# Optimization experiments

Measured on AMD Instinct MI355X. Metric: run time of the kernel, lower is better.

Reference implementation:

```python
import jax, jax.numpy as jnp
import numpy as np

NEG_INF = 1e10  # module's self.inf


def setup_inputs() -> dict:
    key = jax.random.key(0)
    k1, k2, k3, k4 = jax.random.split(key, 4)
    B, To, Ti, d = 16, 2048, 2048, 64
    q = jax.random.normal(k1, (B, To, d), dtype=jnp.float32)
    k = jax.random.normal(k2, (B, Ti, d), dtype=jnp.float32)
    v = jax.random.normal(k3, (B, Ti, d), dtype=jnp.float32)
    prod_mask = jax.random.randint(k4, (B, To, Ti), 0, 2, dtype=jnp.int32)
    return {"q": q, "k": k, "v": v, "prod_mask": prod_mask}


def reference(q, k, v, prod_mask):
    d_qk = q.shape[2]
    # [B, To, Ti] scores
    scaled_qk = jnp.einsum('bod,bid->boi', q, k) / jnp.sqrt(jnp.float32(d_qk))
    scaled_qk = jnp.where(prod_mask == 0, jnp.float32(-NEG_INF), scaled_qk)
    weights = jax.nn.softmax(scaled_qk, axis=2)
    # v flattened over trailing dims is already [B, Ti, d] here
    attended_v = jnp.einsum('boi,bid->bod', weights, v)
    return attended_v
```

## Files before the change

### kernel.cpp

```cpp
#include <hip/hip_runtime.h>
#include <stdint.h>

#define BATCH 16
#define TO 2048
#define TI 2048
#define DH 64
#define NITER2 16

typedef __attribute__((ext_vector_type(8))) short bf16x8;
typedef __attribute__((ext_vector_type(4))) float f32x4;

__device__ __forceinline__ unsigned short f2bf(float f) {
  uint32_t x = __float_as_uint(f);
  x += 0x7fffu + ((x >> 16) & 1u);
  return (unsigned short)(x >> 16);
}

__global__ __launch_bounds__(256) void convert_kv(
    const float* __restrict__ kg, const float* __restrict__ vg,
    unsigned short* __restrict__ k_bf, unsigned short* __restrict__ v_t) {
  __shared__ __align__(16) unsigned short vt[64][72];
  int b = blockIdx.y;
  int i0 = blockIdx.x * 64;
  int t = threadIdx.x;

  {
    const float4* src = (const float4*)(kg + ((size_t)b * TI + i0) * DH);
    ushort4* dst = (ushort4*)(k_bf + ((size_t)b * TI + i0) * DH);
#pragma unroll
    for (int u = 0; u < 4; ++u) {
      float4 f = src[t + 256 * u];
      ushort4 o;
      o.x = f2bf(f.x); o.y = f2bf(f.y); o.z = f2bf(f.z); o.w = f2bf(f.w);
      dst[t + 256 * u] = o;
    }
  }
  {
    const float4* src = (const float4*)(vg + ((size_t)b * TI + i0) * DH);
#pragma unroll
    for (int u = 0; u < 4; ++u) {
      int idx = t + 256 * u;
      int row = idx >> 4;
      int c4 = idx & 15;
      float4 f = src[idx];
      vt[c4 * 4 + 0][row] = f2bf(f.x);
      vt[c4 * 4 + 1][row] = f2bf(f.y);
      vt[c4 * 4 + 2][row] = f2bf(f.z);
      vt[c4 * 4 + 3][row] = f2bf(f.w);
    }
  }
  __syncthreads();
  {
    int dd = t >> 2, part = t & 3;
    ushort4* dst = (ushort4*)(v_t + ((size_t)b * DH + dd) * TI + i0 + part * 16);
#pragma unroll
    for (int u = 0; u < 4; ++u) {
      ushort4 o;
      o.x = vt[dd][part * 16 + u * 4 + 0];
      o.y = vt[dd][part * 16 + u * 4 + 1];
      o.z = vt[dd][part * 16 + u * 4 + 2];
      o.w = vt[dd][part * 16 + u * 4 + 3];
      dst[u] = o;
    }
  }
}

#define ATTN_BODY(IC, MCUR, MNXT)                                              \
  {                                                                            \
    if ((IC) < NITER2 - 1) {                                                   \
      _Pragma("unroll") for (int mt = 0; mt < 4; ++mt)                         \
          MNXT[mt] = *(const int4*)(mbase + mt * 16);                          \
      mbase += 64;                                                             \
    }                                                                          \
                                        \
    f32x4 st[4];                                                               \
    _Pragma("unroll") for (int mt = 0; mt < 4; ++mt) {                         \
      bf16x8 kf0 = *(const bf16x8*)&k_lds[g][mt * 16 + ln15][quad * 8];        \
      bf16x8 kf1 = *(const bf16x8*)&k_lds[g][mt * 16 + ln15][32 + quad * 8];   \
      f32x4 acc = (f32x4){0.f, 0.f, 0.f, 0.f};                                 \
      acc = __builtin_amdgcn_mfma_f32_16x16x32_bf16(kf0, qf[0], acc, 0, 0, 0); \
      acc = __builtin_amdgcn_mfma_f32_16x16x32_bf16(kf1, qf[1], acc, 0, 0, 0); \
      st[mt] = acc;                                                            \
    }                                                                          \
         \
    _Pragma("unroll") for (int mt = 0; mt < 4; ++mt) {                         \
      float p0 = (MCUR[mt].x != 0) ? __expf(st[mt][0]) : 0.f;                  \
      float p1 = (MCUR[mt].y != 0) ? __expf(st[mt][1]) : 0.f;                  \
      float p2 = (MCUR[mt].z != 0) ? __expf(st[mt][2]) : 0.f;                  \
      float p3 = (MCUR[mt].w != 0) ? __expf(st[mt][3]) : 0.f;                  \
      l_part += (p0 + p1) + (p2 + p3);                                         \
      uint32_t lo = (uint32_t)f2bf(p0) | ((uint32_t)f2bf(p1) << 16);           \
      uint32_t hi = (uint32_t)f2bf(p2) | ((uint32_t)f2bf(p3) << 16);           \
      uint2 pk; pk.x = lo; pk.y = hi;                                          \
      *(uint2*)&p_row[wave][ln15][mt * 16 + quad * 4] = pk;                    \
    }                                                                          \
            \
    bf16x8 pf0 = *(const bf16x8*)&p_row[wave][ln15][quad * 8];                 \
    bf16x8 pf1 = *(const bf16x8*)&p_row[wave][ln15][32 + quad * 8];            \
                                                         \
    _Pragma("unroll") for (int dt = 0; dt < 4; ++dt) {                         \
      bf16x8 vf0 = *(const bf16x8*)&v_lds[g][dt * 16 + ln15][quad * 8];        \
      bf16x8 vf1 = *(const bf16x8*)&v_lds[g][dt * 16 + ln15][32 + quad * 8];   \
      o_acc[dt] = __builtin_amdgcn_mfma_f32_16x16x32_bf16(vf0, pf0, o_acc[dt], 0, 0, 0); \
      o_acc[dt] = __builtin_amdgcn_mfma_f32_16x16x32_bf16(vf1, pf1, o_acc[dt], 0, 0, 0); \
    }                                                                          \
                                          \
    asm volatile("s_waitcnt lgkmcnt(0)\n\ts_barrier" ::: "memory");            \
    if ((IC) < NITER2 - 1) {                                                   \
                        \
      *(uint4*)&k_lds[g][row][part * 16] = ka0;                                \
      *(uint4*)&k_lds[g][row][part * 16 + 8] = ka1;                            \
      *(uint4*)&v_lds[g][row][part * 16] = va0;                                \
      *(uint4*)&v_lds[g][row][part * 16 + 8] = va1;                            \
               \
      if ((IC) < NITER2 - 2) {                                                 \
        ka0 = kp[0]; ka1 = kp[1];                                              \
        va0 = vp[0]; va1 = vp[1];                                              \
        kp = (const uint4*)((const char*)kp + 64 * DH * 2);                    \
        vp = (const uint4*)((const char*)vp + 64 * 2);                         \
      }                                                                        \
                                    \
      asm volatile("s_waitcnt lgkmcnt(0)\n\ts_barrier" ::: "memory");          \
    }                                                                          \
  }

__global__ __launch_bounds__(512) void attn_kernel(
    const float* __restrict__ q, const int* __restrict__ mask,
    const unsigned short* __restrict__ k_bf, const unsigned short* __restrict__ v_t,
    float* __restrict__ out) {
  __shared__ __align__(16) unsigned short k_lds[2][64][72];
  __shared__ __align__(16) unsigned short v_lds[2][64][72];
  __shared__ __align__(16) unsigned short p_row[8][16][72];

  int n = blockIdx.x;
  int xcd = n & 7;
  int slot = n >> 3;
  int b = (xcd << 1) | (slot >> 5);
  int o_blk = slot & 31;

  int t = threadIdx.x;
  int wave = t >> 6;
  int g = wave >> 2;
  int w = wave & 3;
  int lane = t & 63;
  int ln15 = lane & 15;
  int quad = lane >> 4;

  int qrow = o_blk * 64 + w * 16 + ln15;

  bf16x8 qf[2];
  {
    const float* qp = q + ((size_t)b * TO + qrow) * DH;
#pragma unroll
    for (int kc = 0; kc < 2; ++kc) {
      int kk = kc * 32 + quad * 8;
      float4 f0 = *(const float4*)(qp + kk);
      float4 f1 = *(const float4*)(qp + kk + 4);
      bf16x8 a;
      a[0] = (short)f2bf(f0.x * 0.125f);
      a[1] = (short)f2bf(f0.y * 0.125f);
      a[2] = (short)f2bf(f0.z * 0.125f);
      a[3] = (short)f2bf(f0.w * 0.125f);
      a[4] = (short)f2bf(f1.x * 0.125f);
      a[5] = (short)f2bf(f1.y * 0.125f);
      a[6] = (short)f2bf(f1.z * 0.125f);
      a[7] = (short)f2bf(f1.w * 0.125f);
      qf[kc] = a;
    }
  }

  f32x4 o_acc[4];
#pragma unroll
  for (int dt = 0; dt < 4; ++dt) o_acc[dt] = (f32x4){0.f, 0.f, 0.f, 0.f};
  float l_part = 0.f;

  int tg = t & 255;
  int row = tg >> 2, part = tg & 3;
  const uint4* kp = (const uint4*)(k_bf + ((size_t)b * TI + g * 1024 + row) * DH + part * 16);
  const uint4* vp = (const uint4*)(v_t + ((size_t)b * DH + row) * TI + g * 1024 + part * 16);
  const int* mbase = mask + ((size_t)b * TO + qrow) * TI + g * 1024 + quad * 4;

  uint4 ka0 = kp[0], ka1 = kp[1];
  uint4 va0 = vp[0], va1 = vp[1];
  kp = (const uint4*)((const char*)kp + 64 * DH * 2);
  vp = (const uint4*)((const char*)vp + 64 * 2);
  *(uint4*)&k_lds[g][row][part * 16] = ka0;
  *(uint4*)&k_lds[g][row][part * 16 + 8] = ka1;
  *(uint4*)&v_lds[g][row][part * 16] = va0;
  *(uint4*)&v_lds[g][row][part * 16 + 8] = va1;
  ka0 = kp[0]; ka1 = kp[1];
  va0 = vp[0]; va1 = vp[1];
  kp = (const uint4*)((const char*)kp + 64 * DH * 2);
  vp = (const uint4*)((const char*)vp + 64 * 2);
  int4 mv[4], mw[4];
#pragma unroll
  for (int mt = 0; mt < 4; ++mt) mv[mt] = *(const int4*)(mbase + mt * 16);
  mbase += 64;
  asm volatile("s_waitcnt lgkmcnt(0)\n\ts_barrier" ::: "memory");

  for (int ic = 0; ic < NITER2; ic += 2) {
    ATTN_BODY(ic, mv, mw)
    ATTN_BODY(ic + 1, mw, mv)
  }

  l_part += __shfl_xor(l_part, 16);
  l_part += __shfl_xor(l_part, 32);

  float* scr = (float*)&k_lds[0][0][0];
  float* lscr = (float*)&p_row[0][0][0];
  int orow_i = w * 16 + ln15;

  if (g == 1) {
#pragma unroll
    for (int dt = 0; dt < 4; ++dt)
      *(f32x4*)&scr[(size_t)orow_i * 68 + dt * 16 + quad * 4] = o_acc[dt];
    if (quad == 0) lscr[orow_i] = l_part;
  }
  asm volatile("s_waitcnt lgkmcnt(0)\n\ts_barrier" ::: "memory");
  if (g == 0) {
    float inv = 1.0f / (l_part + lscr[orow_i]);
    float* orow = out + ((size_t)b * TO + qrow) * DH;
#pragma unroll
    for (int dt = 0; dt < 4; ++dt) {
      f32x4 other = *(const f32x4*)&scr[(size_t)orow_i * 68 + dt * 16 + quad * 4];
      float4 vout;
      vout.x = (o_acc[dt][0] + other[0]) * inv;
      vout.y = (o_acc[dt][1] + other[1]) * inv;
      vout.z = (o_acc[dt][2] + other[2]) * inv;
      vout.w = (o_acc[dt][3] + other[3]) * inv;
      *(float4*)(orow + dt * 16 + quad * 4) = vout;
    }
  }
}

extern "C" void kernel_launch(void* const* d_in, const int* in_sizes, int n_in,
                              void* d_out, int out_size, void* d_ws, size_t ws_size,
                              hipStream_t stream) {
  const float* q = (const float*)d_in[0];
  const float* k = (const float*)d_in[1];
  const float* v = (const float*)d_in[2];
  const int* mask = (const int*)d_in[3];

  unsigned short* k_bf = (unsigned short*)d_ws;
  unsigned short* v_t = k_bf + (size_t)BATCH * TI * DH;

  convert_kv<<<dim3(TI / 64, BATCH), 256, 0, stream>>>(k, v, k_bf, v_t);
  attn_kernel<<<dim3(TO / 64 * BATCH), 512, 0, stream>>>(q, mask, k_bf, v_t, (float*)d_out);
}
```

Before: 90.86 us.

## Double-buffer K/V tiles in LDS with XOR swizzle, one barrier per step

Makes the K and V shared-memory tiles double-buffered, so the next tile is written into the other buffer while the current one is read. This drops the second barrier per iteration and moves the global prefetch earlier. It replaces the padded 72-wide rows with a 64-wide XOR-swizzled layout for K, V and P, keeping bank-conflict avoidance while using less LDS, and adds a min-blocks hint to launch bounds. LDS use grows from the extra buffer, and the launch-bounds hint may constrain register allocation.

```diff
diff --git a/kernel.cpp b/kernel.cpp
--- a/kernel.cpp
+++ b/kernel.cpp
@@ -65,18 +65,36 @@
   }
 }
 
-#define ATTN_BODY(IC, MCUR, MNXT)                                              \
+#define ATTN_BODY(CUR, IC, MCUR, MNXT)                                         \
   {                                                                            \
     if ((IC) < NITER2 - 1) {                                                   \
       _Pragma("unroll") for (int mt = 0; mt < 4; ++mt)                         \
           MNXT[mt] = *(const int4*)(mbase + mt * 16);                          \
       mbase += 64;                                                             \
-    }                                                                          \
-                                        \
+         \
+      {                                                                        \
+        unsigned short* kd = &k_lds[g][(CUR) ^ 1][row][0];                     \
+        unsigned short* vd = &v_lds[g][(CUR) ^ 1][row][0];                     \
+        int h = row & 7;                                                       \
+        *(uint4*)(kd + ((((2 * part) ^ h) << 3))) = ka0;                       \
+        *(uint4*)(kd + ((((2 * part + 1) ^ h) << 3))) = ka1;                   \
+        *(uint4*)(vd + ((((2 * part) ^ h) << 3))) = va0;                       \
+        *(uint4*)(vd + ((((2 * part + 1) ^ h) << 3))) = va1;                   \
+      }                                                                        \
+    }                                                                          \
+                \
+    if ((IC) < NITER2 - 2) {                                                   \
+      ka0 = kp[0]; ka1 = kp[1];                                                \
+      va0 = vp[0]; va1 = vp[1];                                                \
+      kp = (const uint4*)((const char*)kp + 64 * DH * 2);                      \
+      vp = (const uint4*)((const char*)vp + 64 * 2);                           \
+    }                                                                          \
+                 \
     f32x4 st[4];                                                               \
     _Pragma("unroll") for (int mt = 0; mt < 4; ++mt) {                         \
-      bf16x8 kf0 = *(const bf16x8*)&k_lds[g][mt * 16 + ln15][quad * 8];        \
-      bf16x8 kf1 = *(const bf16x8*)&k_lds[g][mt * 16 + ln15][32 + quad * 8];   \
+      const unsigned short* kr = &k_lds[g][CUR][mt * 16 + ln15][0];            \
+      bf16x8 kf0 = *(const bf16x8*)(kr + ((quad ^ hq) << 3));                  \
+      bf16x8 kf1 = *(const bf16x8*)(kr + (((4 + quad) ^ hq) << 3));            \
       f32x4 acc = (f32x4){0.f, 0.f, 0.f, 0.f};                                 \
       acc = __builtin_amdgcn_mfma_f32_16x16x32_bf16(kf0, qf[0], acc, 0, 0, 0); \
       acc = __builtin_amdgcn_mfma_f32_16x16x32_bf16(kf1, qf[1], acc, 0, 0, 0); \
@@ -92,45 +110,31 @@
       uint32_t lo = (uint32_t)f2bf(p0) | ((uint32_t)f2bf(p1) << 16);           \
       uint32_t hi = (uint32_t)f2bf(p2) | ((uint32_t)f2bf(p3) << 16);           \
       uint2 pk; pk.x = lo; pk.y = hi;                                          \
-      *(uint2*)&p_row[wave][ln15][mt * 16 + quad * 4] = pk;                    \
+      *(uint2*)&p_row[wave][ln15][(((2 * mt + (quad >> 1)) ^ hq) << 3) +       \
+                                  ((quad & 1) << 2)] = pk;                     \
     }                                                                          \
             \
-    bf16x8 pf0 = *(const bf16x8*)&p_row[wave][ln15][quad * 8];                 \
-    bf16x8 pf1 = *(const bf16x8*)&p_row[wave][ln15][32 + quad * 8];            \
-                                                         \
+    bf16x8 pf0 = *(const bf16x8*)&p_row[wave][ln15][(quad ^ hq) << 3];         \
+    bf16x8 pf1 = *(const bf16x8*)&p_row[wave][ln15][((4 + quad) ^ hq) << 3];   \
+                                             \
     _Pragma("unroll") for (int dt = 0; dt < 4; ++dt) {                         \
-      bf16x8 vf0 = *(const bf16x8*)&v_lds[g][dt * 16 + ln15][quad * 8];        \
-      bf16x8 vf1 = *(const bf16x8*)&v_lds[g][dt * 16 + ln15][32 + quad * 8];   \
+      const unsigned short* vr = &v_lds[g][CUR][dt * 16 + ln15][0];            \
+      bf16x8 vf0 = *(const bf16x8*)(vr + ((quad ^ hq) << 3));                  \
+      bf16x8 vf1 = *(const bf16x8*)(vr + (((4 + quad) ^ hq) << 3));            \
       o_acc[dt] = __builtin_amdgcn_mfma_f32_16x16x32_bf16(vf0, pf0, o_acc[dt], 0, 0, 0); \
       o_acc[dt] = __builtin_amdgcn_mfma_f32_16x16x32_bf16(vf1, pf1, o_acc[dt], 0, 0, 0); \
     }                                                                          \
-                                          \
+                   \
     asm volatile("s_waitcnt lgkmcnt(0)\n\ts_barrier" ::: "memory");            \
-    if ((IC) < NITER2 - 1) {                                                   \
-                        \
-      *(uint4*)&k_lds[g][row][part * 16] = ka0;                                \
-      *(uint4*)&k_lds[g][row][part * 16 + 8] = ka1;                            \
-      *(uint4*)&v_lds[g][row][part * 16] = va0;                                \
-      *(uint4*)&v_lds[g][row][part * 16 + 8] = va1;                            \
-               \
-      if ((IC) < NITER2 - 2) {                                                 \
-        ka0 = kp[0]; ka1 = kp[1];                                              \
-        va0 = vp[0]; va1 = vp[1];                                              \
-        kp = (const uint4*)((const char*)kp + 64 * DH * 2);                    \
-        vp = (const uint4*)((const char*)vp + 64 * 2);                         \
-      }                                                                        \
-                                    \
-      asm volatile("s_waitcnt lgkmcnt(0)\n\ts_barrier" ::: "memory");          \
-    }                                                                          \
-  }
-
-__global__ __launch_bounds__(512) void attn_kernel(
+  }
+
+__global__ __launch_bounds__(512, 4) void attn_kernel(
     const float* __restrict__ q, const int* __restrict__ mask,
     const unsigned short* __restrict__ k_bf, const unsigned short* __restrict__ v_t,
     float* __restrict__ out) {
-  __shared__ __align__(16) unsigned short k_lds[2][64][72];
-  __shared__ __align__(16) unsigned short v_lds[2][64][72];
-  __shared__ __align__(16) unsigned short p_row[8][16][72];
+  __shared__ __align__(16) unsigned short k_lds[2][2][64][64];
+  __shared__ __align__(16) unsigned short v_lds[2][2][64][64];
+  __shared__ __align__(16) unsigned short p_row[8][16][64];
 
   int n = blockIdx.x;
   int xcd = n & 7;
@@ -145,6 +149,7 @@
   int lane = t & 63;
   int ln15 = lane & 15;
   int quad = lane >> 4;
+  int hq = ln15 & 7;
 
   int qrow = o_blk * 64 + w * 16 + ln15;
 
@@ -184,10 +189,15 @@
   uint4 va0 = vp[0], va1 = vp[1];
   kp = (const uint4*)((const char*)kp + 64 * DH * 2);
   vp = (const uint4*)((const char*)vp + 64 * 2);
-  *(uint4*)&k_lds[g][row][part * 16] = ka0;
-  *(uint4*)&k_lds[g][row][part * 16 + 8] = ka1;
-  *(uint4*)&v_lds[g][row][part * 16] = va0;
-  *(uint4*)&v_lds[g][row][part * 16 + 8] = va1;
+  {
+    unsigned short* kd = &k_lds[g][0][row][0];
+    unsigned short* vd = &v_lds[g][0][row][0];
+    int h = row & 7;
+    *(uint4*)(kd + (((2 * part) ^ h) << 3)) = ka0;
+    *(uint4*)(kd + (((2 * part + 1) ^ h) << 3)) = ka1;
+    *(uint4*)(vd + (((2 * part) ^ h) << 3)) = va0;
+    *(uint4*)(vd + (((2 * part + 1) ^ h) << 3)) = va1;
+  }
   ka0 = kp[0]; ka1 = kp[1];
   va0 = vp[0]; va1 = vp[1];
   kp = (const uint4*)((const char*)kp + 64 * DH * 2);
@@ -199,14 +209,14 @@
   asm volatile("s_waitcnt lgkmcnt(0)\n\ts_barrier" ::: "memory");
 
   for (int ic = 0; ic < NITER2; ic += 2) {
-    ATTN_BODY(ic, mv, mw)
-    ATTN_BODY(ic + 1, mw, mv)
+    ATTN_BODY(0, ic, mv, mw)
+    ATTN_BODY(1, ic + 1, mw, mv)
   }
 
   l_part += __shfl_xor(l_part, 16);
   l_part += __shfl_xor(l_part, 32);
 
-  float* scr = (float*)&k_lds[0][0][0];
+  float* scr = (float*)&k_lds[0][0][0][0];
   float* lscr = (float*)&p_row[0][0][0];
   int orow_i = w * 16 + ln15;
 
```

New measurement: 81.29 us. 1.12x faster.
